# Performance work log

Measured on AMD Instinct MI355X. Metric: run time of the kernel, lower is better.

The kernel has to match this reference:

```python
import jax, jax.numpy as jnp
import numpy as np

C_M, C_Z, NO_BINS = 256, 128, 15
MIN_BIN, MAX_BIN, INF = 3.25, 20.75, 1e8
LN_EPS = 1e-5


def _layer_norm(t, w, b):
    mu = jnp.mean(t, axis=-1, keepdims=True)
    var = jnp.var(t, axis=-1, keepdims=True)
    return (t - mu) * jax.lax.rsqrt(var + LN_EPS) * w + b


def setup_inputs() -> dict:
    key = jax.random.key(0)
    ks = jax.random.split(key, 8)
    B, N = 1, 768
    m = jax.random.normal(ks[0], (B, N, C_M), dtype=jnp.float32)
    z = jax.random.normal(ks[1], (B, N, N, C_Z), dtype=jnp.float32)
    # scale coords so pairwise distances span the 3.25-20.75 A bin range
    x = jax.random.normal(ks[2], (B, N, 3), dtype=jnp.float32) * 10.0
    seqs = jax.random.normal(ks[3], (B, N, 21), dtype=jnp.float32)
    lin_w = jax.random.normal(ks[4], (C_Z, NO_BINS), dtype=jnp.float32) * 0.1
    lin_b = jnp.zeros((C_Z,), dtype=jnp.float32)
    ln_m_w = jnp.ones((C_M,), dtype=jnp.float32)
    ln_m_b = jnp.zeros((C_M,), dtype=jnp.float32)
    ln_z_w = jnp.ones((C_Z,), dtype=jnp.float32)
    ln_z_b = jnp.zeros((C_Z,), dtype=jnp.float32)
    return {"m": m, "z": z, "x": x, "seqs": seqs,
            "lin_w": lin_w, "lin_b": lin_b,
            "ln_m_w": ln_m_w, "ln_m_b": ln_m_b,
            "ln_z_w": ln_z_w, "ln_z_b": ln_z_b}


def reference(m, z, x, seqs, lin_w, lin_b, ln_m_w, ln_m_b, ln_z_w, ln_z_b):
    # m update: LayerNorm only (track_seq_states=False, seqs unused)
    m_update = _layer_norm(m, ln_m_w, ln_m_b)

    bins = jnp.linspace(MIN_BIN, MAX_BIN, NO_BINS, dtype=x.dtype)
    sq_bins = bins ** 2
    upper = jnp.concatenate([sq_bins[1:], jnp.array([INF], dtype=x.dtype)])

    # pairwise squared distances [*, N, N, 1]
    diff = x[..., :, None, :] - x[..., None, :, :]
    d = jnp.sum(diff ** 2, axis=-1, keepdims=True)
    # one-hot distogram [*, N, N, no_bins] (strict inequalities, matching torch)
    oh = ((d > sq_bins) & (d < upper)).astype(x.dtype)
    # Linear(no_bins -> c_z)
    d_emb = jnp.einsum('...b,cb->...c', oh, lin_w) + lin_b

    z_update = d_emb + _layer_norm(z, ln_z_w, ln_z_b)
    return (m_update, z_update)
```

## Files before the change

### kernel.cpp

```cpp
#include <hip/hip_runtime.h>

#define LN_EPS 1e-5f
#define C_M 256
#define C_Z 128
#define NO_BINS 15

typedef float f4 __attribute__((ext_vector_type(4)));

__device__ __forceinline__ f4 f4zero() { f4 t = {0.f, 0.f, 0.f, 0.f}; return t; }

__device__ __forceinline__ int bin_of(const float* __restrict__ x,
                                      const float* sqb, int i, int j)
{
    const float dx = x[3 * i + 0] - x[3 * j + 0];
    const float dy = x[3 * i + 1] - x[3 * j + 1];
    const float dz = x[3 * i + 2] - x[3 * j + 2];
    const float d = __fadd_rn(__fadd_rn(__fmul_rn(dx, dx), __fmul_rn(dy, dy)),
                              __fmul_rn(dz, dz));
    int cnt = 0;
#pragma unroll
    for (int k = 0; k < NO_BINS; ++k) {
        const float bk = 3.25f + 1.25f * (float)k;
        cnt += (d > bk * bk) ? 1 : 0;
    }
    return ((cnt > 0) && (d < 1e8f) && (d != sqb[cnt])) ? cnt - 1 : -1;
}

__global__ __launch_bounds__(256) void fused_kernel(
    const float* __restrict__ m, const float* __restrict__ ln_m_w,
    const float* __restrict__ ln_m_b, float* __restrict__ out_m, int m_rows,
    const float* __restrict__ z, const float* __restrict__ x,
    const float* __restrict__ lin_w, const float* __restrict__ lin_b,
    const float* __restrict__ ln_z_w, const float* __restrict__ ln_z_b,
    float* __restrict__ out_z, int N, int di, int rem)
{
    __shared__ float lw[NO_BINS * C_Z];
    __shared__ float sqb[16];
    const int tid = threadIdx.x;
    for (int t = tid; t < NO_BINS * C_Z; t += 256) {
        const int c = t / NO_BINS;
        const int bin = t - c * NO_BINS;
        lw[bin * C_Z + c] = lin_w[t];
    }
    if (tid < 16) {
        const float bk = 3.25f + 1.25f * (float)tid;
        sqb[tid] = (tid < NO_BINS) ? bk * bk : -1.0f;
    }
    __syncthreads();

    if ((int)blockIdx.x < ((m_rows + 3) >> 2)) {
        const int wid    = tid >> 6;
        const int lane64 = tid & 63;
        const int row    = blockIdx.x * 4 + wid;
        if (row < m_rows) {
            const f4 v = reinterpret_cast<const f4*>(m + (long long)row * C_M)[lane64];
            float s  = v.x + v.y + v.z + v.w;
            float s2 = v.x * v.x + v.y * v.y + v.z * v.z + v.w * v.w;
#pragma unroll
            for (int msk = 1; msk < 64; msk <<= 1) {
                s  += __shfl_xor(s,  msk);
                s2 += __shfl_xor(s2, msk);
            }
            const float mu  = s * (1.0f / C_M);
            const float inv = rsqrtf(s2 * (1.0f / C_M) - mu * mu + LN_EPS);
            const f4 wv = reinterpret_cast<const f4*>(ln_m_w)[lane64];
            const f4 bv = reinterpret_cast<const f4*>(ln_m_b)[lane64];
            f4 o = (v - mu) * inv * wv + bv;
            reinterpret_cast<f4*>(out_m + (long long)row * C_M)[lane64] = o;
        }
    }

    const int half = tid >> 5;
    const int lane = tid & 31;

    const f4 wv = reinterpret_cast<const f4*>(ln_z_w)[lane];
    f4 bv = reinterpret_cast<const f4*>(ln_z_b)[lane];
    bv += reinterpret_cast<const f4*>(lin_b)[lane];

    const long long total  = (long long)N * N;
    const long long stride = (long long)gridDim.x * 8;

    long long r = (long long)blockIdx.x * 8 + half;
    int i = (int)(r / N);
    int j = (int)(r - (long long)i * N);

    for (; r < total; r += 2 * stride) {
        const long long ra = r;
        const long long rb = r + stride;
        const bool hb = rb < total;

        const int ia = i, ja = j;
        int ib = i + di, jb = j + rem;
        if (jb >= N) { jb -= N; ib += 1; }
        i = ib + di; j = jb + rem;
        if (j >= N) { j -= N; i += 1; }

        const f4 va = reinterpret_cast<const f4*>(z + ra * C_Z)[lane];
        f4 vb = f4zero();
        if (hb) vb = reinterpret_cast<const f4*>(z + rb * C_Z)[lane];

        const int bina = bin_of(x, sqb, ia, ja);
        const int binb = hb ? bin_of(x, sqb, ib, jb) : -1;

        f4 ea = f4zero(), eb = f4zero();
        if (bina >= 0) ea = reinterpret_cast<const f4*>(lw + bina * C_Z)[lane];
        if (binb >= 0) eb = reinterpret_cast<const f4*>(lw + binb * C_Z)[lane];

        float sa  = va.x + va.y + va.z + va.w;
        float s2a = va.x * va.x + va.y * va.y + va.z * va.z + va.w * va.w;
        float sb  = vb.x + vb.y + vb.z + vb.w;
        float s2b = vb.x * vb.x + vb.y * vb.y + vb.z * vb.z + vb.w * vb.w;
#pragma unroll
        for (int msk = 1; msk < 32; msk <<= 1) {
            sa  += __shfl_xor(sa,  msk);
            s2a += __shfl_xor(s2a, msk);
            sb  += __shfl_xor(sb,  msk);
            s2b += __shfl_xor(s2b, msk);
        }
        const float mua  = sa * (1.0f / C_Z);
        const float inva = rsqrtf(s2a * (1.0f / C_Z) - mua * mua + LN_EPS);
        const float mub  = sb * (1.0f / C_Z);
        const float invb = rsqrtf(s2b * (1.0f / C_Z) - mub * mub + LN_EPS);

        f4 oa = (va - mua) * inva * wv + bv + ea;
        __builtin_nontemporal_store(oa, reinterpret_cast<f4*>(out_z + ra * C_Z) + lane);
        if (hb) {
            f4 ob = (vb - mub) * invb * wv + bv + eb;
            __builtin_nontemporal_store(ob, reinterpret_cast<f4*>(out_z + rb * C_Z) + lane);
        }
    }
}

extern "C" void kernel_launch(void* const* d_in, const int* in_sizes, int n_in,
                              void* d_out, int out_size, void* d_ws, size_t ws_size,
                              hipStream_t stream) {
    const float* m      = (const float*)d_in[0];
    const float* z      = (const float*)d_in[1];
    const float* x      = (const float*)d_in[2];
    const float* lin_w  = (const float*)d_in[4];
    const float* lin_b  = (const float*)d_in[5];
    const float* ln_m_w = (const float*)d_in[6];
    const float* ln_m_b = (const float*)d_in[7];
    const float* ln_z_w = (const float*)d_in[8];
    const float* ln_z_b = (const float*)d_in[9];

    const int N = in_sizes[0] / C_M;
    float* out_m = (float*)d_out;
    float* out_z = out_m + (long long)N * C_M;

    const int gcd8 = (N % 8 == 0) ? 8 : (N % 4 == 0) ? 4 : (N % 2 == 0) ? 2 : 1;
    const int unit = N / gcd8;
    int g = (4608 / unit) * unit;
    if (g <= 0) g = unit;
    const int mB = (N + 3) / 4;
    if (g < mB) g = ((mB + unit - 1) / unit) * unit;

    const long long stride = (long long)g * 8;
    const int di  = (int)(stride / N);
    const int rem = (int)(stride % N);

    fused_kernel<<<g, 256, 0, stream>>>(m, ln_m_w, ln_m_b, out_m, N,
                                        z, x, lin_w, lin_b, ln_z_w, ln_z_b,
                                        out_z, N, di, rem);
}
```

Baseline: 116.1 us.

## Add uniform-grid kernel with fixed column per half-wave and 4-row unroll

When N is a multiple of 16, a specialised kernel runs with 2N blocks. Each half-wave keeps a fixed column j, loads that column's coordinates once, and steps through rows i by 16. It keeps four z rows in flight per iteration, removing the per-iteration index arithmetic and bounds checks, and raising memory-level parallelism. It sets launch_bounds for 6 blocks per CU. Any other N falls back to a simpler generic grid-stride kernel.

```diff
diff --git a/kernel.cpp b/kernel.cpp
--- a/kernel.cpp
+++ b/kernel.cpp
@@ -9,12 +9,13 @@
 
 __device__ __forceinline__ f4 f4zero() { f4 t = {0.f, 0.f, 0.f, 0.f}; return t; }
 
-__device__ __forceinline__ int bin_of(const float* __restrict__ x,
-                                      const float* sqb, int i, int j)
-{
-    const float dx = x[3 * i + 0] - x[3 * j + 0];
-    const float dy = x[3 * i + 1] - x[3 * j + 1];
-    const float dz = x[3 * i + 2] - x[3 * j + 2];
+__device__ __forceinline__ int bin_of_xj(const float* __restrict__ x,
+                                         const float* sqb, int i,
+                                         float xj0, float xj1, float xj2)
+{
+    const float dx = x[3 * i + 0] - xj0;
+    const float dy = x[3 * i + 1] - xj1;
+    const float dz = x[3 * i + 2] - xj2;
     const float d = __fadd_rn(__fadd_rn(__fmul_rn(dx, dx), __fmul_rn(dy, dy)),
                               __fmul_rn(dz, dz));
     int cnt = 0;
@@ -26,13 +27,19 @@
     return ((cnt > 0) && (d < 1e8f) && (d != sqb[cnt])) ? cnt - 1 : -1;
 }
 
-__global__ __launch_bounds__(256) void fused_kernel(
+__device__ __forceinline__ void ln_stats(const f4 v, float& s, float& s2)
+{
+    s  = v.x + v.y + v.z + v.w;
+    s2 = v.x * v.x + v.y * v.y + v.z * v.z + v.w * v.w;
+}
+
+__global__ __launch_bounds__(256, 6) void fused_uniform(
     const float* __restrict__ m, const float* __restrict__ ln_m_w,
     const float* __restrict__ ln_m_b, float* __restrict__ out_m, int m_rows,
     const float* __restrict__ z, const float* __restrict__ x,
     const float* __restrict__ lin_w, const float* __restrict__ lin_b,
     const float* __restrict__ ln_z_w, const float* __restrict__ ln_z_b,
-    float* __restrict__ out_z, int N, int di, int rem)
+    float* __restrict__ out_z, int N, int iters)
 {
     __shared__ float lw[NO_BINS * C_Z];
     __shared__ float sqb[16];
@@ -54,8 +61,7 @@
         const int row    = blockIdx.x * 4 + wid;
         if (row < m_rows) {
             const f4 v = reinterpret_cast<const f4*>(m + (long long)row * C_M)[lane64];
-            float s  = v.x + v.y + v.z + v.w;
-            float s2 = v.x * v.x + v.y * v.y + v.z * v.z + v.w * v.w;
+            float s, s2; ln_stats(v, s, s2);
 #pragma unroll
             for (int msk = 1; msk < 64; msk <<= 1) {
                 s  += __shfl_xor(s,  msk);
@@ -77,57 +83,139 @@
     f4 bv = reinterpret_cast<const f4*>(ln_z_b)[lane];
     bv += reinterpret_cast<const f4*>(lin_b)[lane];
 
+    const int slot = (int)blockIdx.x * 8 + half;
+    const long long stride = (long long)N * 16;
+    int i = slot / N;
+    const int j = slot - i * N;
+
+    const float xj0 = x[3 * j + 0];
+    const float xj1 = x[3 * j + 1];
+    const float xj2 = x[3 * j + 2];
+
+    long long r = slot;
+    for (int t = 0; t < iters; t += 4) {
+        const long long r0 = r, r1 = r + stride, r2 = r + 2 * stride, r3 = r + 3 * stride;
+        const int i0 = i, i1 = i + 16, i2 = i + 32, i3 = i + 48;
+
+        const f4 v0 = reinterpret_cast<const f4*>(z + r0 * C_Z)[lane];
+        const f4 v1 = reinterpret_cast<const f4*>(z + r1 * C_Z)[lane];
+        const f4 v2 = reinterpret_cast<const f4*>(z + r2 * C_Z)[lane];
+        const f4 v3 = reinterpret_cast<const f4*>(z + r3 * C_Z)[lane];
+
+        const int b0 = bin_of_xj(x, sqb, i0, xj0, xj1, xj2);
+        const int b1 = bin_of_xj(x, sqb, i1, xj0, xj1, xj2);
+        const int b2 = bin_of_xj(x, sqb, i2, xj0, xj1, xj2);
+        const int b3 = bin_of_xj(x, sqb, i3, xj0, xj1, xj2);
+
+        f4 e0 = f4zero(), e1 = f4zero(), e2 = f4zero(), e3 = f4zero();
+        if (b0 >= 0) e0 = reinterpret_cast<const f4*>(lw + b0 * C_Z)[lane];
+        if (b1 >= 0) e1 = reinterpret_cast<const f4*>(lw + b1 * C_Z)[lane];
+        if (b2 >= 0) e2 = reinterpret_cast<const f4*>(lw + b2 * C_Z)[lane];
+        if (b3 >= 0) e3 = reinterpret_cast<const f4*>(lw + b3 * C_Z)[lane];
+
+        float s0, q0, s1, q1, s2, q2, s3, q3;
+        ln_stats(v0, s0, q0); ln_stats(v1, s1, q1);
+        ln_stats(v2, s2, q2); ln_stats(v3, s3, q3);
+#pragma unroll
+        for (int msk = 1; msk < 32; msk <<= 1) {
+            s0 += __shfl_xor(s0, msk); q0 += __shfl_xor(q0, msk);
+            s1 += __shfl_xor(s1, msk); q1 += __shfl_xor(q1, msk);
+            s2 += __shfl_xor(s2, msk); q2 += __shfl_xor(q2, msk);
+            s3 += __shfl_xor(s3, msk); q3 += __shfl_xor(q3, msk);
+        }
+        const float mu0 = s0 * (1.0f / C_Z), iv0 = rsqrtf(q0 * (1.0f / C_Z) - mu0 * mu0 + LN_EPS);
+        const float mu1 = s1 * (1.0f / C_Z), iv1 = rsqrtf(q1 * (1.0f / C_Z) - mu1 * mu1 + LN_EPS);
+        const float mu2 = s2 * (1.0f / C_Z), iv2 = rsqrtf(q2 * (1.0f / C_Z) - mu2 * mu2 + LN_EPS);
+        const float mu3 = s3 * (1.0f / C_Z), iv3 = rsqrtf(q3 * (1.0f / C_Z) - mu3 * mu3 + LN_EPS);
+
+        f4 o0 = (v0 - mu0) * iv0 * wv + bv + e0;
+        f4 o1 = (v1 - mu1) * iv1 * wv + bv + e1;
+        f4 o2 = (v2 - mu2) * iv2 * wv + bv + e2;
+        f4 o3 = (v3 - mu3) * iv3 * wv + bv + e3;
+        __builtin_nontemporal_store(o0, reinterpret_cast<f4*>(out_z + r0 * C_Z) + lane);
+        __builtin_nontemporal_store(o1, reinterpret_cast<f4*>(out_z + r1 * C_Z) + lane);
+        __builtin_nontemporal_store(o2, reinterpret_cast<f4*>(out_z + r2 * C_Z) + lane);
+        __builtin_nontemporal_store(o3, reinterpret_cast<f4*>(out_z + r3 * C_Z) + lane);
+
+        r += 4 * stride;
+        i += 64;
+    }
+}
+
+__device__ __forceinline__ int bin_of(const float* __restrict__ x,
+                                      const float* sqb, int i, int j)
+{
+    return bin_of_xj(x, sqb, i, x[3 * j], x[3 * j + 1], x[3 * j + 2]);
+}
+
+__global__ __launch_bounds__(256) void fused_generic(
+    const float* __restrict__ m, const float* __restrict__ ln_m_w,
+    const float* __restrict__ ln_m_b, float* __restrict__ out_m, int m_rows,
+    const float* __restrict__ z, const float* __restrict__ x,
+    const float* __restrict__ lin_w, const float* __restrict__ lin_b,
+    const float* __restrict__ ln_z_w, const float* __restrict__ ln_z_b,
+    float* __restrict__ out_z, int N)
+{
+    __shared__ float lw[NO_BINS * C_Z];
+    __shared__ float sqb[16];
+    const int tid = threadIdx.x;
+    for (int t = tid; t < NO_BINS * C_Z; t += 256) {
+        const int c = t / NO_BINS;
+        const int bin = t - c * NO_BINS;
+        lw[bin * C_Z + c] = lin_w[t];
+    }
+    if (tid < 16) {
+        const float bk = 3.25f + 1.25f * (float)tid;
+        sqb[tid] = (tid < NO_BINS) ? bk * bk : -1.0f;
+    }
+    __syncthreads();
+
+    if ((int)blockIdx.x < ((m_rows + 3) >> 2)) {
+        const int wid    = tid >> 6;
+        const int lane64 = tid & 63;
+        const int row    = blockIdx.x * 4 + wid;
+        if (row < m_rows) {
+            const f4 v = reinterpret_cast<const f4*>(m + (long long)row * C_M)[lane64];
+            float s, s2; ln_stats(v, s, s2);
+#pragma unroll
+            for (int msk = 1; msk < 64; msk <<= 1) {
+                s  += __shfl_xor(s,  msk);
+                s2 += __shfl_xor(s2, msk);
+            }
+            const float mu  = s * (1.0f / C_M);
+            const float inv = rsqrtf(s2 * (1.0f / C_M) - mu * mu + LN_EPS);
+            const f4 wv = reinterpret_cast<const f4*>(ln_m_w)[lane64];
+            const f4 bv = reinterpret_cast<const f4*>(ln_m_b)[lane64];
+            f4 o = (v - mu) * inv * wv + bv;
+            reinterpret_cast<f4*>(out_m + (long long)row * C_M)[lane64] = o;
+        }
+    }
+
+    const int half = tid >> 5;
+    const int lane = tid & 31;
+    const f4 wv = reinterpret_cast<const f4*>(ln_z_w)[lane];
+    f4 bv = reinterpret_cast<const f4*>(ln_z_b)[lane];
+    bv += reinterpret_cast<const f4*>(lin_b)[lane];
+
     const long long total  = (long long)N * N;
     const long long stride = (long long)gridDim.x * 8;
-
-    long long r = (long long)blockIdx.x * 8 + half;
-    int i = (int)(r / N);
-    int j = (int)(r - (long long)i * N);
-
-    for (; r < total; r += 2 * stride) {
-        const long long ra = r;
-        const long long rb = r + stride;
-        const bool hb = rb < total;
-
-        const int ia = i, ja = j;
-        int ib = i + di, jb = j + rem;
-        if (jb >= N) { jb -= N; ib += 1; }
-        i = ib + di; j = jb + rem;
-        if (j >= N) { j -= N; i += 1; }
-
-        const f4 va = reinterpret_cast<const f4*>(z + ra * C_Z)[lane];
-        f4 vb = f4zero();
-        if (hb) vb = reinterpret_cast<const f4*>(z + rb * C_Z)[lane];
-
-        const int bina = bin_of(x, sqb, ia, ja);
-        const int binb = hb ? bin_of(x, sqb, ib, jb) : -1;
-
-        f4 ea = f4zero(), eb = f4zero();
-        if (bina >= 0) ea = reinterpret_cast<const f4*>(lw + bina * C_Z)[lane];
-        if (binb >= 0) eb = reinterpret_cast<const f4*>(lw + binb * C_Z)[lane];
-
-        float sa  = va.x + va.y + va.z + va.w;
-        float s2a = va.x * va.x + va.y * va.y + va.z * va.z + va.w * va.w;
-        float sb  = vb.x + vb.y + vb.z + vb.w;
-        float s2b = vb.x * vb.x + vb.y * vb.y + vb.z * vb.z + vb.w * vb.w;
+    for (long long r = (long long)blockIdx.x * 8 + half; r < total; r += stride) {
+        const int i = (int)(r / N);
+        const int j = (int)(r - (long long)i * N);
+        const f4 v = reinterpret_cast<const f4*>(z + r * C_Z)[lane];
+        const int bin = bin_of(x, sqb, i, j);
+        f4 e = f4zero();
+        if (bin >= 0) e = reinterpret_cast<const f4*>(lw + bin * C_Z)[lane];
+        float s, s2; ln_stats(v, s, s2);
 #pragma unroll
         for (int msk = 1; msk < 32; msk <<= 1) {
-            sa  += __shfl_xor(sa,  msk);
-            s2a += __shfl_xor(s2a, msk);
-            sb  += __shfl_xor(sb,  msk);
-            s2b += __shfl_xor(s2b, msk);
-        }
-        const float mua  = sa * (1.0f / C_Z);
-        const float inva = rsqrtf(s2a * (1.0f / C_Z) - mua * mua + LN_EPS);
-        const float mub  = sb * (1.0f / C_Z);
-        const float invb = rsqrtf(s2b * (1.0f / C_Z) - mub * mub + LN_EPS);
-
-        f4 oa = (va - mua) * inva * wv + bv + ea;
-        __builtin_nontemporal_store(oa, reinterpret_cast<f4*>(out_z + ra * C_Z) + lane);
-        if (hb) {
-            f4 ob = (vb - mub) * invb * wv + bv + eb;
-            __builtin_nontemporal_store(ob, reinterpret_cast<f4*>(out_z + rb * C_Z) + lane);
-        }
+            s  += __shfl_xor(s,  msk);
+            s2 += __shfl_xor(s2, msk);
+        }
+        const float mu  = s * (1.0f / C_Z);
+        const float inv = rsqrtf(s2 * (1.0f / C_Z) - mu * mu + LN_EPS);
+        f4 o = (v - mu) * inv * wv + bv + e;
+        __builtin_nontemporal_store(o, reinterpret_cast<f4*>(out_z + r * C_Z) + lane);
     }
 }
 
@@ -148,18 +236,16 @@
     float* out_m = (float*)d_out;
     float* out_z = out_m + (long long)N * C_M;
 
-    const int gcd8 = (N % 8 == 0) ? 8 : (N % 4 == 0) ? 4 : (N % 2 == 0) ? 2 : 1;
-    const int unit = N / gcd8;
-    int g = (4608 / unit) * unit;
-    if (g <= 0) g = unit;
-    const int mB = (N + 3) / 4;
-    if (g < mB) g = ((mB + unit - 1) / unit) * unit;
-
-    const long long stride = (long long)g * 8;
-    const int di  = (int)(stride / N);
-    const int rem = (int)(stride % N);
-
-    fused_kernel<<<g, 256, 0, stream>>>(m, ln_m_w, ln_m_b, out_m, N,
-                                        z, x, lin_w, lin_b, ln_z_w, ln_z_b,
-                                        out_z, N, di, rem);
-}
+    if ((N % 16) == 0 && 2 * N >= (N + 3) / 4) {
+        fused_uniform<<<2 * N, 256, 0, stream>>>(m, ln_m_w, ln_m_b, out_m, N,
+                                                 z, x, lin_w, lin_b, ln_z_w, ln_z_b,
+                                                 out_z, N, N / 16);
+    } else {
+        int g = 2048;
+        const int mB = (N + 3) / 4;
+        if (g < mB) g = mB;
+        fused_generic<<<g, 256, 0, stream>>>(m, ln_m_w, ln_m_b, out_m, N,
+                                             z, x, lin_w, lin_b, ln_z_w, ln_z_b,
+                                             out_z, N);
+    }
+}
```

After: 109.9 us. -5.3%, faster.
